# Kernel tuning notes

Measured on AMD Instinct MI355X. Metric: run time of the kernel, lower is better.

Reference implementation:

```python
import jax, jax.numpy as jnp
import numpy as np

BS, NQ, NK = 4096, 21, 7   # batch, num_neg queries, 7 keys (weekdays)
E = 512                     # key_size == query_size
H = 512                     # hidden_size
NEG_INF = -1e9


def setup_inputs() -> dict:
    key = jax.random.key(0)
    ks = jax.random.split(key, 6)
    sq = 1.0 / np.sqrt(E)
    sh = 1.0 / np.sqrt(H)
    return {
        "queries": jax.random.normal(ks[0], (BS, NQ, E), jnp.float32),
        "keys": jax.random.normal(ks[1], (BS, NK, E), jnp.float32),
        "wq_w": jax.random.normal(ks[2], (H, E), jnp.float32) * sq,
        "wq_b": jnp.zeros((H,), jnp.float32),
        "wk_w": jax.random.normal(ks[3], (H, E), jnp.float32) * sq,
        "wk_b": jnp.zeros((H,), jnp.float32),
        "wv_w": jax.random.normal(ks[4], (1, H), jnp.float32) * sh,
        "wv_b": jnp.zeros((1,), jnp.float32),
        "cum_subs_masks": jax.random.randint(ks[5], (BS, 1, NK, 1), 0, 2).astype(jnp.int32),
        "num_neg": NQ,
    }


def reference(queries, keys, wq_w, wq_b, wk_w, wk_b, wv_w, wv_b, cum_subs_masks, num_neg):
    # dropout p=0.0 -> identity (as in eval / p=0)
    q = jnp.einsum('bqe,he->bqh', queries, wq_w) + wq_b          # (bs,21,H)
    k = jnp.einsum('bke,he->bkh', keys, wk_w) + wk_b             # (bs,7,H)
    # additive score: broadcast q over keys, k over queries
    t = jnp.tanh(q[:, :, None, :] + k[:, None, :, :])            # (bs,21,7,H)
    scores = jnp.einsum('bqkh,oh->bqko', t, wv_w) + wv_b         # (bs,21,7,1)
    scores = scores + cum_subs_masks.astype(scores.dtype) * NEG_INF
    attn_weights = jax.nn.softmax(scores, axis=-2)               # softmax over 7 keys
    # weighted sum of the RAW keys (the module multiplies by expanded `keys`)
    attn_out = jnp.einsum('bqk,bke->bqe', attn_weights[..., 0], keys)  # (bs,21,E)
    return (attn_out, attn_weights)
```

## Files before the change

### kernel.cpp

```cpp
#include <hip/hip_runtime.h>
#include <hip/hip_bf16.h>

#define BS_   4096
#define NQ_   21
#define NK_   7
#define E_    512
#define MQ_   (BS_*NQ_)
#define MK_   (BS_*NK_)
#define MTQ_  (MQ_/64)
#define MTT_  ((MQ_+MK_)/64)
#define SCALE_ 2.88539008177792681f

typedef __attribute__((ext_vector_type(8))) short bf16x8;
typedef __attribute__((ext_vector_type(4))) float f32x4;
typedef __attribute__((ext_vector_type(8))) unsigned short u16x8;

__device__ __forceinline__ unsigned int cvt_pk_bf16(float lo, float hi){
  unsigned int r;
  asm("v_cvt_pk_bf16_f32 %0, %1, %2" : "=v"(r) : "v"(lo), "v"(hi));
  return r;
}
__device__ __forceinline__ float bf2f(unsigned short h){
  return __builtin_bit_cast(float, (unsigned int)h << 16);
}

__global__ __launch_bounds__(256) void cast_weights(
    const float* __restrict__ wq, const float* __restrict__ wk,
    unsigned int* __restrict__ oq, unsigned int* __restrict__ ok)
{
  int i = blockIdx.x * 256 + threadIdx.x;
  float4 a = ((const float4*)wq)[i];
  float4 b = ((const float4*)wk)[i];
  uint2 ua = { cvt_pk_bf16(a.x, a.y), cvt_pk_bf16(a.z, a.w) };
  uint2 ub = { cvt_pk_bf16(b.x, b.y), cvt_pk_bf16(b.z, b.w) };
  ((uint2*)oq)[i] = ua;
  ((uint2*)ok)[i] = ub;
}

__global__ __launch_bounds__(256)
void gemm_proj(const float* __restrict__ Aq, const float* __restrict__ Ak,
               const unsigned short* __restrict__ Bq, const unsigned short* __restrict__ Bk,
               const float* __restrict__ bq, const float* __restrict__ bk,
               unsigned short* __restrict__ Cq, unsigned short* __restrict__ Ck)
{
  __shared__ char Asm[64 * 1024];

  const int tid  = threadIdx.x;
  const int lane = tid & 63;
  const int w    = tid >> 6;
  const int l15  = lane & 15;
  const int s4   = lane >> 4;

  const int orig = (int)blockIdx.x;
  int mt = (orig & 7) * (MTT_ / 8) + (orig >> 3);

  const float* A; const unsigned short* Bw; const float* bias; unsigned short* C;
  if (mt < MTQ_){ A = Aq; Bw = Bq; bias = bq; C = Cq; }
  else          { A = Ak; Bw = Bk; bias = bk; C = Ck; mt -= MTQ_; }

  const long m0  = (long)mt << 6;
  const int  n0w = w << 7;
  const char* Abyte = (const char*)(A + m0 * E_);

  const unsigned short* Bpn[8];
#pragma unroll
  for (int n = 0; n < 8; ++n)
    Bpn[n] = Bw + (long)(n0w + n * 16 + l15) * E_ + s4 * 8;

  int aoffE[4], aoffO[4];
#pragma unroll
  for (int m = 0; m < 4; ++m){
    const int r  = m * 16 + l15;
    const int b2 = (r >> 2) & 1;
    const int bs = r * 1024 + ((s4 ^ (r & 3)) << 4);
    aoffE[m] = bs + b2 * 64;
    aoffO[m] = bs - b2 * 64;
  }

  f32x4 acc[4][8];
  const f32x4 z4 = {0.f, 0.f, 0.f, 0.f};
#pragma unroll
  for (int m = 0; m < 4; ++m)
#pragma unroll
    for (int n = 0; n < 8; ++n) acc[m][n] = z4;

  bf16x8 b0[8], b1[8];

#pragma unroll
  for (int n = 0; n < 8; ++n)
    b0[n] = *(const bf16x8*)((const char*)Bpn[n]);

#define AISSUE(buf, g) do { \
  _Pragma("unroll") for (int ii = 0; ii < 8; ++ii){ \
    const int c_ = tid + ((g) * 8 + ii) * 256; \
    buf[ii] = *(const float4*)(Abyte + (long)(c_ >> 7) * 2048 + (c_ & 127) * 16); \
  } \
} while(0)
#define AWRITE(buf, g) do { \
  _Pragma("unroll") for (int ii = 0; ii < 8; ++ii){ \
    const int c_ = tid + ((g) * 8 + ii) * 256; \
    const int row_ = c_ >> 7, sl_ = c_ & 127; \
    uint2 u_ = { cvt_pk_bf16(buf[ii].x, buf[ii].y), cvt_pk_bf16(buf[ii].z, buf[ii].w) }; \
    *(uint2*)(Asm + row_ * 1024 + (((sl_ >> 1) ^ (row_ & 7)) << 4) + (sl_ & 1) * 8) = u_; \
  } \
} while(0)

  {
    float4 avX[8], avY[8];
    AISSUE(avX, 0);
    AISSUE(avY, 1);
    AWRITE(avX, 0);
    AISSUE(avX, 2);
    AWRITE(avY, 1);
    AISSUE(avY, 3);
    AWRITE(avX, 2);
    AWRITE(avY, 3);
  }
  __syncthreads();

#define KSTEP(T, BCUR, BNXT) do { \
  if ((T) < 15){ \
    _Pragma("unroll") for (int n_ = 0; n_ < 8; ++n_) \
      BNXT[n_] = *(const bf16x8*)((const char*)Bpn[n_] + ((T) + 1) * 64); \
  } \
  bf16x8 af_[4]; \
  _Pragma("unroll") for (int m_ = 0; m_ < 4; ++m_) \
    af_[m_] = *(const bf16x8*)(Asm + (((T) & 1) ? aoffO[m_] : aoffE[m_]) + (T) * 64); \
  _Pragma("unroll") for (int m_ = 0; m_ < 4; ++m_) \
    _Pragma("unroll") for (int n_ = 0; n_ < 8; ++n_) \
      acc[m_][n_] = __builtin_amdgcn_mfma_f32_16x16x32_bf16(af_[m_], BCUR[n_], acc[m_][n_], 0, 0, 0); \
} while(0)

#pragma unroll
  for (int tp = 0; tp < 8; ++tp){
    KSTEP(2 * tp,     b0, b1);
    KSTEP(2 * tp + 1, b1, b0);
  }

#undef AISSUE
#undef AWRITE
#undef KSTEP

  const int ccol0 = n0w + l15;
  float bvs[8];
#pragma unroll
  for (int n = 0; n < 8; ++n) bvs[n] = bias[ccol0 + n * 16] * SCALE_;
#pragma unroll
  for (int m = 0; m < 4; ++m){
    const long rbase = m0 + m * 16 + s4 * 4;
#pragma unroll
    for (int n = 0; n < 8; ++n){
      const long col = ccol0 + n * 16;
      float v0 = fmaf(acc[m][n][0], SCALE_, bvs[n]);
      float v1 = fmaf(acc[m][n][1], SCALE_, bvs[n]);
      float v2 = fmaf(acc[m][n][2], SCALE_, bvs[n]);
      float v3 = fmaf(acc[m][n][3], SCALE_, bvs[n]);
      unsigned int u01 = cvt_pk_bf16(v0, v1);
      unsigned int u23 = cvt_pk_bf16(v2, v3);
      C[(rbase + 0) * E_ + col] = (unsigned short)(u01 & 0xffffu);
      C[(rbase + 1) * E_ + col] = (unsigned short)(u01 >> 16);
      C[(rbase + 2) * E_ + col] = (unsigned short)(u23 & 0xffffu);
      C[(rbase + 3) * E_ + col] = (unsigned short)(u23 >> 16);
    }
  }
}

__global__ __launch_bounds__(256, 2)
void attn_fused(const unsigned short* __restrict__ qp,
                const unsigned short* __restrict__ kp,
                const float* __restrict__ keys,
                const float* __restrict__ wv, const float* __restrict__ wvb,
                const int* __restrict__ mask,
                float* __restrict__ out0, float* __restrict__ out1)
{
  const int lane = threadIdx.x & 63;
  const int b    = blockIdx.x * 4 + (threadIdx.x >> 6);

  float wvr[8];
  *(float4*)&wvr[0] = ((const float4*)wv)[lane * 2];
  *(float4*)&wvr[4] = ((const float4*)wv)[lane * 2 + 1];

  float kf[NK_][8];
#pragma unroll
  for (int k = 0; k < NK_; ++k){
    u16x8 u = *(const u16x8*)(kp + ((long)b * NK_ + k) * E_ + lane * 8);
#pragma unroll
    for (int j = 0; j < 8; ++j) kf[k][j] = bf2f((unsigned short)u[j]);
  }
  float kr[NK_][8];
#pragma unroll
  for (int k = 0; k < NK_; ++k){
    const float4* p = (const float4*)(keys + ((long)b * NK_ + k) * E_ + lane * 8);
    *(float4*)&kr[k][0] = p[0];
    *(float4*)&kr[k][4] = p[1];
  }

  float wsum = ((wvr[0] + wvr[1]) + (wvr[2] + wvr[3])) + ((wvr[4] + wvr[5]) + (wvr[6] + wvr[7]));
#pragma unroll
  for (int off = 32; off; off >>= 1) wsum += __shfl_xor(wsum, off, 64);

  const float vb = wvb[0];
  float base[NK_];
#pragma unroll
  for (int k = 0; k < NK_; ++k)
    base[k] = (wsum + vb) + (float)mask[b * NK_ + k] * (-1e9f);

  const unsigned short* qrow = qp + (long)b * NQ_ * E_ + lane * 8;
  u16x8 qv = *(const u16x8*)qrow;

  float4* o0 = (float4*)(out0 + (long)b * NQ_ * E_) + lane * 2;
  float*  o1 = out1 + (long)b * (NQ_ * NK_);

  for (int qi = 0; qi < NQ_; ++qi){
    u16x8 qn = qv;
    if (qi < NQ_ - 1) qn = *(const u16x8*)(qrow + (qi + 1) * E_);

    float qf[8];
#pragma unroll
    for (int j = 0; j < 8; ++j) qf[j] = bf2f((unsigned short)qv[j]);
    qv = qn;

    float acc[NK_];
#pragma unroll
    for (int k = 0; k < NK_; ++k){
      float a = 0.f;
#pragma unroll
      for (int j = 0; j < 8; ++j){
        float x = qf[j] + kf[k][j];
        float e = __builtin_amdgcn_exp2f(x);
        float r = __builtin_amdgcn_rcpf(e + 1.0f);
        a = fmaf(wvr[j], r, a);
      }
      acc[k] = a;
    }
#pragma unroll
    for (int k = 0; k < NK_; ++k){
      float a = acc[k];
#pragma unroll
      for (int off = 32; off; off >>= 1) a += __shfl_xor(a, off, 64);
      acc[k] = a;
    }
    float sc[NK_], mx = -3.4e38f;
#pragma unroll
    for (int k = 0; k < NK_; ++k){ sc[k] = fmaf(-2.f, acc[k], base[k]); mx = fmaxf(mx, sc[k]); }
    float sum = 0.f;
#pragma unroll
    for (int k = 0; k < NK_; ++k){ sc[k] = __expf(sc[k] - mx); sum += sc[k]; }
    const float inv = __builtin_amdgcn_rcpf(sum);
    float wgt[NK_];
#pragma unroll
    for (int k = 0; k < NK_; ++k) wgt[k] = sc[k] * inv;

    float wsel = wgt[0];
#pragma unroll
    for (int k = 1; k < NK_; ++k) wsel = (lane == k) ? wgt[k] : wsel;
    if (lane < NK_) o1[qi * NK_ + lane] = wsel;

    float4 lo = {0.f,0.f,0.f,0.f}, hi = {0.f,0.f,0.f,0.f};
#pragma unroll
    for (int k = 0; k < NK_; ++k){
      lo.x = fmaf(wgt[k], kr[k][0], lo.x);
      lo.y = fmaf(wgt[k], kr[k][1], lo.y);
      lo.z = fmaf(wgt[k], kr[k][2], lo.z);
      lo.w = fmaf(wgt[k], kr[k][3], lo.w);
      hi.x = fmaf(wgt[k], kr[k][4], hi.x);
      hi.y = fmaf(wgt[k], kr[k][5], hi.y);
      hi.z = fmaf(wgt[k], kr[k][6], hi.z);
      hi.w = fmaf(wgt[k], kr[k][7], hi.w);
    }
    o0[qi * 128 + 0] = lo;
    o0[qi * 128 + 1] = hi;
  }
}

extern "C" void kernel_launch(void* const* d_in, const int* in_sizes, int n_in,
                              void* d_out, int out_size, void* d_ws, size_t ws_size,
                              hipStream_t stream)
{
  const float* queries = (const float*)d_in[0];
  const float* keys    = (const float*)d_in[1];
  const float* wq_w    = (const float*)d_in[2];
  const float* wq_b    = (const float*)d_in[3];
  const float* wk_w    = (const float*)d_in[4];
  const float* wk_b    = (const float*)d_in[5];
  const float* wv_w    = (const float*)d_in[6];
  const float* wv_b    = (const float*)d_in[7];
  const int*   mask    = (const int*)d_in[8];
  (void)in_sizes; (void)n_in; (void)out_size; (void)ws_size;

  float* out0 = (float*)d_out;
  float* out1 = out0 + (long)MQ_ * E_;

  char* ws = (char*)d_ws;
  unsigned short* wqb = (unsigned short*)ws;
  unsigned short* wkb = (unsigned short*)(ws + 512 * 512 * 2);
  unsigned short* qb  = (unsigned short*)(ws + (1 << 20));
  unsigned short* kb  = qb + (size_t)MQ_ * E_;

  cast_weights<<<dim3(256), dim3(256), 0, stream>>>(wq_w, wk_w, (unsigned int*)wqb, (unsigned int*)wkb);
  gemm_proj<<<dim3(MTT_), dim3(256), 0, stream>>>(
      queries, keys, wqb, wkb, wq_b, wk_b, qb, kb);
  attn_fused<<<dim3(BS_ / 4), dim3(256), 0, stream>>>(qb, kb, keys, wv_w, wv_b, mask, out0, out1);
}
```

Before: 289.9 us.

## Retile projection GEMM to 256x128 with double-buffered direct global-to-LDS loads

Changes the projection GEMM from a 64-row by full-width tile to 256-row by 128-column tiles with a 2D block mapping. Instead of staging the full A row-panel once and reading B straight from global memory, it double-buffers K slices of fp32 A and bf16 B through LDS using global_load_lds. fp32 A is now converted to bf16 at fragment read time. The aim is to overlap the loads with MFMA work and raise operand reuse. In exchange, each A element is converted once per column tile, the kernel uses 80KB of LDS, and it syncs once per K step.

```diff
diff --git a/kernel.cpp b/kernel.cpp
--- a/kernel.cpp
+++ b/kernel.cpp
@@ -7,8 +7,8 @@
 #define E_    512
 #define MQ_   (BS_*NQ_)
 #define MK_   (BS_*NK_)
-#define MTQ_  (MQ_/64)
-#define MTT_  ((MQ_+MK_)/64)
+#define MTQ_  (MQ_/256)
+#define MTT_  ((MQ_+MK_)/256)
 #define SCALE_ 2.88539008177792681f
 
 typedef __attribute__((ext_vector_type(8))) short bf16x8;
@@ -20,8 +20,16 @@
   asm("v_cvt_pk_bf16_f32 %0, %1, %2" : "=v"(r) : "v"(lo), "v"(hi));
   return r;
 }
+__device__ __forceinline__ unsigned short f2bfu(float x){
+  return __builtin_bit_cast(unsigned short, __float2bfloat16(x));
+}
 __device__ __forceinline__ float bf2f(unsigned short h){
   return __builtin_bit_cast(float, (unsigned int)h << 16);
+}
+__device__ __forceinline__ void gload_lds16(const void* g, void* l){
+  __builtin_amdgcn_global_load_lds(
+      (const __attribute__((address_space(1))) unsigned int*)g,
+      (__attribute__((address_space(3))) unsigned int*)l, 16, 0, 0);
 }
 
 __global__ __launch_bounds__(256) void cast_weights(
@@ -43,7 +51,7 @@
                const float* __restrict__ bq, const float* __restrict__ bk,
                unsigned short* __restrict__ Cq, unsigned short* __restrict__ Ck)
 {
-  __shared__ char Asm[64 * 1024];
+  __shared__ char SH[81920];
 
   const int tid  = threadIdx.x;
   const int lane = tid & 63;
@@ -52,29 +60,49 @@
   const int s4   = lane >> 4;
 
   const int orig = (int)blockIdx.x;
-  int mt = (orig & 7) * (MTT_ / 8) + (orig >> 3);
+  const int xcd  = orig & 7, idx = orig >> 3;
+  int       mt   = xcd * 56 + (idx >> 2);
+  const int nt   = idx & 3;
 
   const float* A; const unsigned short* Bw; const float* bias; unsigned short* C;
   if (mt < MTQ_){ A = Aq; Bw = Bq; bias = bq; C = Cq; }
   else          { A = Ak; Bw = Bk; bias = bk; C = Ck; mt -= MTQ_; }
 
-  const long m0  = (long)mt << 6;
-  const int  n0w = w << 7;
+  const long m0 = (long)mt << 8;
+  const int  n0 = nt << 7;
   const char* Abyte = (const char*)(A + m0 * E_);
-
-  const unsigned short* Bpn[8];
-#pragma unroll
-  for (int n = 0; n < 8; ++n)
-    Bpn[n] = Bw + (long)(n0w + n * 16 + l15) * E_ + s4 * 8;
-
-  int aoffE[4], aoffO[4];
+  const char* Bbyte = (const char*)Bw;
+
+  long asrc[8]; int adst[8];
+#pragma unroll
+  for (int i = 0; i < 8; ++i){
+    const int c   = tid + i * 256;
+    const int row = c >> 3;
+    const int sl  = c & 7;
+    asrc[i] = (long)row * 2048 + ((sl ^ (row & 7)) << 4);
+    adst[i] = c << 4;
+  }
+  long bsrc[2]; int bdst[2];
+#pragma unroll
+  for (int i = 0; i < 2; ++i){
+    const int c   = tid + i * 256;
+    const int row = c >> 2;
+    const int sl  = c & 3;
+    bsrc[i] = (long)(n0 + row) * 1024 + ((sl << 4) ^ (((row >> 1) & 3) << 4));
+    bdst[i] = c << 4;
+  }
+
+  int aoff0[4], aoff1[4], boff[8];
 #pragma unroll
   for (int m = 0; m < 4; ++m){
-    const int r  = m * 16 + l15;
-    const int b2 = (r >> 2) & 1;
-    const int bs = r * 1024 + ((s4 ^ (r & 3)) << 4);
-    aoffE[m] = bs + b2 * 64;
-    aoffO[m] = bs - b2 * 64;
+    const int r = w * 64 + m * 16 + l15;
+    aoff0[m] = r * 128 + (((s4 * 2)     ^ (r & 7)) << 4);
+    aoff1[m] = r * 128 + (((s4 * 2 + 1) ^ (r & 7)) << 4);
+  }
+#pragma unroll
+  for (int n = 0; n < 8; ++n){
+    const int r = n * 16 + l15;
+    boff[n] = r * 64 + ((s4 << 4) ^ (((r >> 1) & 3) << 4));
   }
 
   f32x4 acc[4][8];
@@ -84,70 +112,56 @@
 #pragma unroll
     for (int n = 0; n < 8; ++n) acc[m][n] = z4;
 
-  bf16x8 b0[8], b1[8];
-
-#pragma unroll
-  for (int n = 0; n < 8; ++n)
-    b0[n] = *(const bf16x8*)((const char*)Bpn[n]);
-
-#define AISSUE(buf, g) do { \
-  _Pragma("unroll") for (int ii = 0; ii < 8; ++ii){ \
-    const int c_ = tid + ((g) * 8 + ii) * 256; \
-    buf[ii] = *(const float4*)(Abyte + (long)(c_ >> 7) * 2048 + (c_ & 127) * 16); \
+  union U8 { unsigned short s[8]; bf16x8 v; };
+
+#define STAGE(T, PH) do { \
+  _Pragma("unroll") for (int i_ = 0; i_ < 8; ++i_) \
+    gload_lds16(Abyte + asrc[i_] + (long)(T) * 128, SH + (PH) * 32768 + adst[i_]); \
+  _Pragma("unroll") for (int i_ = 0; i_ < 2; ++i_) \
+    gload_lds16(Bbyte + bsrc[i_] + (T) * 64, SH + 65536 + (PH) * 8192 + bdst[i_]); \
+} while(0)
+
+#define COMPUTE(PH) do { \
+  const char* ab_ = SH + (PH) * 32768; \
+  const char* bb_ = SH + 65536 + (PH) * 8192; \
+  bf16x8 af_[4], bfr_[8]; \
+  _Pragma("unroll") for (int m_ = 0; m_ < 4; ++m_){ \
+    f32x4 lo_ = *(const f32x4*)(ab_ + aoff0[m_]); \
+    f32x4 hi_ = *(const f32x4*)(ab_ + aoff1[m_]); \
+    U8 u_; \
+    u_.s[0] = f2bfu(lo_[0]); u_.s[1] = f2bfu(lo_[1]); \
+    u_.s[2] = f2bfu(lo_[2]); u_.s[3] = f2bfu(lo_[3]); \
+    u_.s[4] = f2bfu(hi_[0]); u_.s[5] = f2bfu(hi_[1]); \
+    u_.s[6] = f2bfu(hi_[2]); u_.s[7] = f2bfu(hi_[3]); \
+    af_[m_] = u_.v; \
   } \
-} while(0)
-#define AWRITE(buf, g) do { \
-  _Pragma("unroll") for (int ii = 0; ii < 8; ++ii){ \
-    const int c_ = tid + ((g) * 8 + ii) * 256; \
-    const int row_ = c_ >> 7, sl_ = c_ & 127; \
-    uint2 u_ = { cvt_pk_bf16(buf[ii].x, buf[ii].y), cvt_pk_bf16(buf[ii].z, buf[ii].w) }; \
-    *(uint2*)(Asm + row_ * 1024 + (((sl_ >> 1) ^ (row_ & 7)) << 4) + (sl_ & 1) * 8) = u_; \
-  } \
-} while(0)
-
-  {
-    float4 avX[8], avY[8];
-    AISSUE(avX, 0);
-    AISSUE(avY, 1);
-    AWRITE(avX, 0);
-    AISSUE(avX, 2);
-    AWRITE(avY, 1);
-    AISSUE(avY, 3);
-    AWRITE(avX, 2);
-    AWRITE(avY, 3);
-  }
-  __syncthreads();
-
-#define KSTEP(T, BCUR, BNXT) do { \
-  if ((T) < 15){ \
-    _Pragma("unroll") for (int n_ = 0; n_ < 8; ++n_) \
-      BNXT[n_] = *(const bf16x8*)((const char*)Bpn[n_] + ((T) + 1) * 64); \
-  } \
-  bf16x8 af_[4]; \
-  _Pragma("unroll") for (int m_ = 0; m_ < 4; ++m_) \
-    af_[m_] = *(const bf16x8*)(Asm + (((T) & 1) ? aoffO[m_] : aoffE[m_]) + (T) * 64); \
+  _Pragma("unroll") for (int n_ = 0; n_ < 8; ++n_) \
+    bfr_[n_] = *(const bf16x8*)(bb_ + boff[n_]); \
   _Pragma("unroll") for (int m_ = 0; m_ < 4; ++m_) \
     _Pragma("unroll") for (int n_ = 0; n_ < 8; ++n_) \
-      acc[m_][n_] = __builtin_amdgcn_mfma_f32_16x16x32_bf16(af_[m_], BCUR[n_], acc[m_][n_], 0, 0, 0); \
+      acc[m_][n_] = __builtin_amdgcn_mfma_f32_16x16x32_bf16(af_[m_], bfr_[n_], acc[m_][n_], 0, 0, 0); \
 } while(0)
 
-#pragma unroll
-  for (int tp = 0; tp < 8; ++tp){
-    KSTEP(2 * tp,     b0, b1);
-    KSTEP(2 * tp + 1, b1, b0);
-  }
-
-#undef AISSUE
-#undef AWRITE
-#undef KSTEP
-
-  const int ccol0 = n0w + l15;
+  STAGE(0, 0);
+  __syncthreads();
+
+#pragma unroll
+  for (int t = 0; t < 16; ++t){
+    if (t < 15) STAGE(t + 1, (t + 1) & 1);
+    COMPUTE(t & 1);
+    __syncthreads();
+  }
+
+#undef STAGE
+#undef COMPUTE
+
+  const int ccol0 = n0 + l15;
   float bvs[8];
 #pragma unroll
   for (int n = 0; n < 8; ++n) bvs[n] = bias[ccol0 + n * 16] * SCALE_;
 #pragma unroll
   for (int m = 0; m < 4; ++m){
-    const long rbase = m0 + m * 16 + s4 * 4;
+    const long rbase = m0 + w * 64 + m * 16 + s4 * 4;
 #pragma unroll
     for (int n = 0; n < 8; ++n){
       const long col = ccol0 + n * 16;
@@ -298,7 +312,7 @@
   unsigned short* kb  = qb + (size_t)MQ_ * E_;
 
   cast_weights<<<dim3(256), dim3(256), 0, stream>>>(wq_w, wk_w, (unsigned int*)wqb, (unsigned int*)wkb);
-  gemm_proj<<<dim3(MTT_), dim3(256), 0, stream>>>(
+  gemm_proj<<<dim3(MTT_ * 4), dim3(256), 0, stream>>>(
       queries, keys, wqb, wkb, wq_b, wk_b, qb, kb);
   attn_fused<<<dim3(BS_ / 4), dim3(256), 0, stream>>>(qb, kb, keys, wv_w, wv_b, mask, out0, out1);
 }
```

Measured after the change: 283.9 us. -2.1%, faster.
